# Kernel tuning notes

Hardware: AMD Instinct MI355X
Metric: run time of the kernel (lower is better)

Reference implementation:

```python
import jax, jax.numpy as jnp
import numpy as np

N, D = 65536, 256


def _unit(x):
    # contrastive embeddings are L2-normalized; also keeps exp(dot) finite
    return x / jnp.linalg.norm(x, axis=-1, keepdims=True)


def setup_inputs() -> dict:
    key = jax.random.key(0)
    k1, k2 = jax.random.split(key)
    z_a = _unit(jax.random.normal(k1, (N, D), dtype=jnp.float32))
    z_b = _unit(jax.random.normal(k2, (N, D), dtype=jnp.float32))
    return {"z_a": z_a, "z_b": z_b}


def reference(z_a, z_b):
    # d_i = dot(z_a[i], z_b[i])  (the only quantity the original ever computes)
    n = z_a.shape[0]
    d = jnp.sum(z_a * z_b, axis=-1)  # [n]
    # Original loop structure:
    #   alignment      = sum_i (-d_i)
    #   negative_sum_i = (# of j in range(n-1), j != i) * d_i
    #                  = (n-2) * d_i for i < n-1, (n-1) * d_i for i == n-1
    #   uniformity_i   = exp(d_i)
    counts = jnp.full((n,), n - 2, dtype=d.dtype).at[n - 1].set(n - 1)
    return jnp.sum((counts - 1.0) * d + jnp.exp(d))
```

## Files before the change

kernel.cpp:

```cpp
#include <hip/hip_runtime.h>
#include <math.h>


#define D_DIM 256
#define ROWS 8
#define BLOCKS 2048

__global__ __launch_bounds__(256, 4)
void dot_loss_partial(const float4* __restrict__ za4,
                      const float4* __restrict__ zb4,
                      float* __restrict__ partial,
                      int n) {
    const int lane = threadIdx.x & 63;
    const int wave = threadIdx.x >> 6;
    const int waveId = blockIdx.x * 4 + wave;
    const int row0 = waveId * ROWS;

    const float4* a = za4 + (size_t)row0 * 64 + lane;
    const float4* b = zb4 + (size_t)row0 * 64 + lane;

    float4 av[ROWS], bv[ROWS];
    #pragma unroll
    for (int r = 0; r < ROWS; ++r) {
        av[r] = a[(size_t)r * 64];
        bv[r] = b[(size_t)r * 64];
    }

    float d[ROWS];
    #pragma unroll
    for (int r = 0; r < ROWS; ++r) {
        float t = av[r].x * bv[r].x;
        t = fmaf(av[r].y, bv[r].y, t);
        t = fmaf(av[r].z, bv[r].z, t);
        t = fmaf(av[r].w, bv[r].w, t);
        d[r] = t;
    }

    #pragma unroll
    for (int off = 32; off > 0; off >>= 1) {
        #pragma unroll
        for (int r = 0; r < ROWS; ++r)
            d[r] += __shfl_down(d[r], off);
    }

    float acc = 0.0f;
    if (lane == 0) {
        #pragma unroll
        for (int r = 0; r < ROWS; ++r) {
            int row = row0 + r;
            float coeff = (row == n - 1) ? (float)(n - 2) : (float)(n - 3);
            acc += coeff * d[r] + expf(d[r]);
        }
    }

    __shared__ float smem[4];
    if (lane == 0) smem[wave] = acc;
    __syncthreads();
    if (threadIdx.x == 0)
        partial[blockIdx.x] = smem[0] + smem[1] + smem[2] + smem[3];
}

__global__ __launch_bounds__(256)
void reduce_partials(const float* __restrict__ partial,
                     float* __restrict__ out,
                     int m) {
    const int lane = threadIdx.x & 63;
    const int wave = threadIdx.x >> 6;
    double s = 0.0;
    for (int i = threadIdx.x; i < m; i += 256)
        s += (double)partial[i];
    #pragma unroll
    for (int off = 32; off > 0; off >>= 1)
        s += __shfl_down(s, off);
    __shared__ double smem[4];
    if (lane == 0) smem[wave] = s;
    __syncthreads();
    if (threadIdx.x == 0)
        out[0] = (float)(smem[0] + smem[1] + smem[2] + smem[3]);
}

extern "C" void kernel_launch(void* const* d_in, const int* in_sizes, int n_in,
                              void* d_out, int out_size, void* d_ws, size_t ws_size,
                              hipStream_t stream) {
    const float4* za4 = (const float4*)d_in[0];
    const float4* zb4 = (const float4*)d_in[1];
    float* out = (float*)d_out;
    float* partial = (float*)d_ws;
    const int n = in_sizes[0] / D_DIM;

    dot_loss_partial<<<BLOCKS, 256, 0, stream>>>(za4, zb4, partial, n);
    reduce_partials<<<1, 256, 0, stream>>>(partial, out, BLOCKS);
}
```

Before: 147.4 us.

## Double-buffer row loads across batches, with fewer blocks covering more rows

Each wave now handles 16 rows in four batches of four. Loads for the next batch are issued before computing the current one, using a two-slot register buffer and a sched_barrier. The grid shrinks to 1024 blocks. The aim is to overlap memory latency with the shuffle reductions, at the cost of fewer waves in flight and partially serialised loads per wave.

Result: no change. 148.5 us (+0.8%).

```diff
diff --git a/kernel.cpp b/kernel.cpp
--- a/kernel.cpp
+++ b/kernel.cpp
@@ -3,8 +3,9 @@
 
 
 #define D_DIM 256
-#define ROWS 8
-#define BLOCKS 2048
+#define BATCH 4
+#define BATCHES 4
+#define BLOCKS 1024
 
 __global__ __launch_bounds__(256, 4)
 void dot_loss_partial(const float4* __restrict__ za4,
@@ -14,42 +15,60 @@
     const int lane = threadIdx.x & 63;
     const int wave = threadIdx.x >> 6;
     const int waveId = blockIdx.x * 4 + wave;
-    const int row0 = waveId * ROWS;
+    const int row0 = waveId * (BATCH * BATCHES);
 
     const float4* a = za4 + (size_t)row0 * 64 + lane;
     const float4* b = zb4 + (size_t)row0 * 64 + lane;
 
-    float4 av[ROWS], bv[ROWS];
-    #pragma unroll
-    for (int r = 0; r < ROWS; ++r) {
-        av[r] = a[(size_t)r * 64];
-        bv[r] = b[(size_t)r * 64];
-    }
-
-    float d[ROWS];
-    #pragma unroll
-    for (int r = 0; r < ROWS; ++r) {
-        float t = av[r].x * bv[r].x;
-        t = fmaf(av[r].y, bv[r].y, t);
-        t = fmaf(av[r].z, bv[r].z, t);
-        t = fmaf(av[r].w, bv[r].w, t);
-        d[r] = t;
-    }
+    float4 av[2][BATCH], bv[2][BATCH];
 
     #pragma unroll
-    for (int off = 32; off > 0; off >>= 1) {
-        #pragma unroll
-        for (int r = 0; r < ROWS; ++r)
-            d[r] += __shfl_down(d[r], off);
+    for (int r = 0; r < BATCH; ++r) {
+        av[0][r] = a[(size_t)r * 64];
+        bv[0][r] = b[(size_t)r * 64];
     }
 
     float acc = 0.0f;
-    if (lane == 0) {
+
+    #pragma unroll
+    for (int batch = 0; batch < BATCHES; ++batch) {
+        const int buf = batch & 1;
+        const int nbuf = buf ^ 1;
+
+        if (batch < BATCHES - 1) {
+            const size_t base = (size_t)(batch + 1) * BATCH * 64;
+            #pragma unroll
+            for (int r = 0; r < BATCH; ++r) {
+                av[nbuf][r] = a[base + (size_t)r * 64];
+                bv[nbuf][r] = b[base + (size_t)r * 64];
+            }
+        }
+        __builtin_amdgcn_sched_barrier(0);
+
+        float d[BATCH];
         #pragma unroll
-        for (int r = 0; r < ROWS; ++r) {
-            int row = row0 + r;
-            float coeff = (row == n - 1) ? (float)(n - 2) : (float)(n - 3);
-            acc += coeff * d[r] + expf(d[r]);
+        for (int r = 0; r < BATCH; ++r) {
+            float t = av[buf][r].x * bv[buf][r].x;
+            t = fmaf(av[buf][r].y, bv[buf][r].y, t);
+            t = fmaf(av[buf][r].z, bv[buf][r].z, t);
+            t = fmaf(av[buf][r].w, bv[buf][r].w, t);
+            d[r] = t;
+        }
+
+        #pragma unroll
+        for (int off = 32; off > 0; off >>= 1) {
+            #pragma unroll
+            for (int r = 0; r < BATCH; ++r)
+                d[r] += __shfl_down(d[r], off);
+        }
+
+        if (lane == 0) {
+            #pragma unroll
+            for (int r = 0; r < BATCH; ++r) {
+                int row = row0 + batch * BATCH + r;
+                float coeff = (row == n - 1) ? (float)(n - 2) : (float)(n - 3);
+                acc += coeff * d[r] + expf(d[r]);
+            }
         }
     }
 
```
